# Performance work log

Measured on AMD Instinct MI355X. Metric: run time of the kernel, lower is better.

The kernel has to match this reference:

```python
import jax, jax.numpy as jnp
import numpy as np

B, C_IN, C_OUT = 32, 64, 128
K_SIZE, STRIDE, PAD, H = 3, 1, 1, 56
H_OUT = (H + 2 * PAD - K_SIZE) // STRIDE + 1


def setup_inputs() -> dict:
    key = jax.random.key(0)
    kx, kw = jax.random.split(key)
    x = jax.random.normal(kx, (B, C_IN, H, H), dtype=jnp.float32)
    # kaiming_uniform-ish init for K of shape [kh, kw, C_in, C_out]
    fan_in = K_SIZE * C_IN * C_OUT  # torch fan_in for this layout (dim1 * receptive field)
    bound = np.sqrt(6.0 / fan_in).astype(np.float32)
    K = jax.random.uniform(kw, (K_SIZE, K_SIZE, C_IN, C_OUT), dtype=jnp.float32,
                           minval=-bound, maxval=bound)
    return {"x": x, "K": K}


def reference(x, K):
    # Faithful to the torch code INCLUDING its mismatched flatten orders:
    #   patch flattened as (C_in, kh, kw); K flattened as (kh, kw, C_in).
    xp = jnp.pad(x, ((0, 0), (0, 0), (PAD, PAD), (PAD, PAD)))
    end = (H_OUT - 1) * STRIDE + 1
    # patches[b, c, di, dj, i, j] = xp[b, c, i*stride+di, j*stride+dj]
    rows = []
    for di in range(K_SIZE):
        cols = []
        for dj in range(K_SIZE):
            cols.append(xp[:, :, di:di + end:STRIDE, dj:dj + end:STRIDE])  # [B,C,Ho,Wo]
        rows.append(jnp.stack(cols, axis=2))  # [B,C,kw,Ho,Wo]
    patches = jnp.stack(rows, axis=2)  # [B, C, kh, kw, Ho, Wo]
    # flatten patch in (C, kh, kw) order -> [B, Ho, Wo, C*kh*kw]
    p = patches.transpose(0, 4, 5, 1, 2, 3).reshape(B, H_OUT, H_OUT, -1)
    # K flattened in (kh, kw, C) order, exactly as K.view(-1, out_channels)
    Kf = K.reshape(-1, C_OUT)  # [kh*kw*C_in, C_out]
    out = p @ Kf  # [B, Ho, Wo, C_out]
    return out.transpose(0, 3, 1, 2)  # [B, C_out, Ho, Wo]
```

## Files before the change

kernel.cpp:

```cpp
#include <hip/hip_runtime.h>
#include <hip/hip_bf16.h>
#include <stdint.h>


#define B_   32
#define CIN  64
#define COUT 128
#define H_   56
#define HP   58
#define F_   576

typedef __attribute__((ext_vector_type(8))) short bf16x8;
typedef __attribute__((ext_vector_type(4))) float f32x4;

#define AS1 __attribute__((address_space(1)))
#define AS3 __attribute__((address_space(3)))

#define XP_ELEMS (B_*HP*HP*CIN)
#define XP_SLACK 4096
#define XP_TOTAL (XP_ELEMS + XP_SLACK)
#define WG_ELEMS (COUT*F_)
#define WS_NEEDED ((size_t)(XP_TOTAL + WG_ELEMS) * 2)

#define NROW   (B_*HP)
#define NWBLK  (WG_ELEMS/256)

#define A_BYTES 44544
#define B_OFF   (2*A_BYTES)
#define LDS_TOT (B_OFF + 64*F_*2)

__device__ __forceinline__ int aswz(int tot) {
  return (tot & ~127) | ((tot & 127) ^ (((tot >> 7) & 7) << 4));
}

__global__ __launch_bounds__(256) void prep_all(const float* __restrict__ x,
                                                const float* __restrict__ K,
                                                __hip_bfloat16* __restrict__ xpT,
                                                __hip_bfloat16* __restrict__ WgT) {
  const int id = blockIdx.x;
  const int t  = threadIdx.x;

  if (id > NROW) {
    int n = (id - (NROW + 1))*256 + t;
    int co = n / F_, g = n % F_;
    int di = g / 192, dj = (g % 192) / 64, c = g & 63;
    int f  = c*9 + di*3 + dj;
    int kh = f / 192, kw = (f % 192) / 64, cc = f & 63;
    WgT[n] = __float2bfloat16(K[(((size_t)kh*3 + kw)*CIN + cc)*COUT + co]);
    return;
  }
  if (id == NROW) {
    bf16x8 z = (bf16x8)0;
    for (int idx = t; idx < XP_SLACK/8; idx += 256)
      ((bf16x8*)(xpT + XP_ELEMS))[idx] = z;
    return;
  }

  const int b = id / HP, h = id % HP;
  __hip_bfloat16* orow = xpT + (size_t)(b*HP + h) * HP * CIN;
  if (h == 0 || h == HP-1) {
    bf16x8 z = (bf16x8)0;
    for (int idx = t; idx < HP*CIN/8; idx += 256) ((bf16x8*)orow)[idx] = z;
    return;
  }
  __shared__ __align__(16) float scr[CIN*64];
  const float* xrow = x + ((size_t)(b*CIN)*H_ + (h-1)) * H_;
  for (int idx = t; idx < CIN*14; idx += 256) {
    int c = idx / 14, w4 = idx % 14;
    f32x4 v = *(const f32x4*)(xrow + (size_t)c*(H_*H_) + w4*4);
    *(f32x4*)&scr[c*64 + ((w4 + (c >> 3)) & 15)*4] = v;
  }
  __syncthreads();
  for (int idx = t; idx < HP*8; idx += 256) {
    int wp = idx >> 3, cg = (idx & 7) * 8;
    __align__(16) __hip_bfloat16 tmp[8];
    if (wp == 0 || wp == HP-1) {
#pragma unroll
      for (int k2 = 0; k2 < 8; ++k2) tmp[k2] = __float2bfloat16(0.f);
    } else {
      int w = wp - 1, sl = w >> 2, off = w & 3;
#pragma unroll
      for (int k2 = 0; k2 < 8; ++k2) {
        int c = cg + k2;
        tmp[k2] = __float2bfloat16(scr[c*64 + ((sl + (c >> 3)) & 15)*4 + off]);
      }
    }
    *(bf16x8*)(orow + (size_t)wp*CIN + cg) = *(const bf16x8*)tmp;
  }
}

__global__ __launch_bounds__(256) void conv_mfma(
    const __hip_bfloat16* __restrict__ xpT,
    const __hip_bfloat16* __restrict__ WgT,
    float* __restrict__ out) {
  __shared__ __align__(16) char lds[LDS_TOT];
  const int t    = threadIdx.x;
  const int wave = t >> 6;
  const int l    = t & 63;
  const int lr   = l & 15, lq = l >> 4;
  const int bid  = blockIdx.x;
  const int ch   = bid & 1;
  const int u    = bid >> 1;
  const int m0   = u*4;

  const char* wh = (const char*)WgT + (size_t)(ch*64)*1152;

#pragma unroll
  for (int s = 0; s < 18; ++s) {
    int o  = s*4096 + t*16;
    int co = o / 1152;
    int rb = o - co*1152;
    __builtin_amdgcn_global_load_lds(
        (const AS1 void*)(wh + co*1152 + (rb ^ ((co & 7) << 4))),
        (AS3 void*)(lds + B_OFF + s*4096 + wave*1024), 16, 0, 0);
  }

  auto stageA = [&](int m, char* buf) {
    int bb = m & 31, itile = m >> 5;
    const char* xb = (const char*)xpT +
        (size_t)(bb*HP + itile*4) * HP * CIN * 2;
#pragma unroll
    for (int s = 0; s < 11; ++s) {
      int off = s*4096 + t*16;
      if (off < A_BYTES)
        __builtin_amdgcn_global_load_lds(
            (const AS1 void*)(xb + aswz(off)),
            (AS3 void*)(buf + s*4096 + wave*1024), 16, 0, 0);
    }
  };

  char* Acur = lds;
  char* Anxt = lds + A_BYTES;
  stageA(m0, Acur);
  asm volatile("s_waitcnt vmcnt(0)" ::: "memory");
  __builtin_amdgcn_s_barrier();
  __builtin_amdgcn_sched_barrier(0);

  for (int k = 0; k < 4; ++k) {
    if (k < 3) stageA(m0 + k + 1, Anxt);
    __builtin_amdgcn_sched_barrier(0);

    f32x4 acc[4][4];
#pragma unroll
    for (int mi = 0; mi < 4; ++mi)
#pragma unroll
      for (int ni = 0; ni < 4; ++ni) acc[mi][ni] = (f32x4)0.f;
#pragma unroll
    for (int hc = 0; hc < 18; ++hc) {
      const int kg  = hc*32;
      const int di  = kg / 192;
      const int rem = kg - di*192;
      bf16x8 a[4], bq[4];
#pragma unroll
      for (int mi = 0; mi < 4; ++mi) {
        int tot = ((wave + di)*HP + mi*16 + lr)*128 + rem*2 + lq*16;
        a[mi] = *(const bf16x8*)(Acur + aswz(tot));
      }
      const int kb = hc*64 + lq*16;
#pragma unroll
      for (int ni = 0; ni < 4; ++ni) {
        int co = ni*16 + lr;
        bq[ni] = *(const bf16x8*)(lds + B_OFF + co*1152 + (kb ^ ((co & 7) << 4)));
      }
      __builtin_amdgcn_s_setprio(1);
#pragma unroll
      for (int mi = 0; mi < 4; ++mi)
#pragma unroll
        for (int ni = 0; ni < 4; ++ni)
          acc[mi][ni] = __builtin_amdgcn_mfma_f32_16x16x32_bf16(
              a[mi], bq[ni], acc[mi][ni], 0, 0, 0);
      __builtin_amdgcn_s_setprio(0);
    }
    __builtin_amdgcn_sched_barrier(0);

    {
      int m = m0 + k, bb = m & 31;
      int i = (m >> 5)*4 + wave;
#pragma unroll
      for (int mi = 0; mi < 4; ++mi) {
        int j0 = mi*16 + lq*4;
#pragma unroll
        for (int ni = 0; ni < 4; ++ni) {
          if (j0 < H_) {
            int co = ch*64 + ni*16 + lr;
            float* dst = out + (((size_t)(bb*COUT + co))*H_ + i)*H_ + j0;
            *(f32x4*)dst = acc[mi][ni];
          }
        }
      }
    }
    if (k < 3) {
      asm volatile("s_waitcnt vmcnt(16)" ::: "memory");
      __builtin_amdgcn_s_barrier();
      __builtin_amdgcn_sched_barrier(0);
      char* tmp = Acur; Acur = Anxt; Anxt = tmp;
    }
  }
}

__global__ __launch_bounds__(256) void conv_naive(const float* __restrict__ x,
                                                  const float* __restrict__ K,
                                                  float* __restrict__ out) {
  int idx = blockIdx.x*256 + threadIdx.x;
  const int total = B_*COUT*H_*H_;
  if (idx >= total) return;
  int j = idx % H_, i = (idx / H_) % H_, co = (idx / (H_*H_)) % COUT, b = idx / (H_*H_*COUT);
  float s = 0.f;
  for (int c = 0; c < CIN; ++c)
    for (int di = 0; di < 3; ++di) {
      int ii = i + di - 1;
      if (ii < 0 || ii >= H_) continue;
      for (int dj = 0; dj < 3; ++dj) {
        int jj = j + dj - 1;
        if (jj < 0 || jj >= H_) continue;
        int f = c*9 + di*3 + dj;
        int kh = f / 192, kw = (f % 192) / 64, cc = f & 63;
        s += x[(((size_t)b*CIN + c)*H_ + ii)*H_ + jj] *
             K[(((size_t)kh*3 + kw)*CIN + cc)*COUT + co];
      }
    }
  out[idx] = s;
}

extern "C" void kernel_launch(void* const* d_in, const int* in_sizes, int n_in,
                              void* d_out, int out_size, void* d_ws, size_t ws_size,
                              hipStream_t stream) {
  const float* x = (const float*)d_in[0];
  const float* K = (const float*)d_in[1];
  float* out = (float*)d_out;
  if (ws_size >= WS_NEEDED) {
    __hip_bfloat16* xpT = (__hip_bfloat16*)d_ws;
    __hip_bfloat16* WgT = xpT + XP_TOTAL;
    prep_all<<<NROW + 1 + NWBLK, 256, 0, stream>>>(x, K, xpT, WgT);
    conv_mfma<<<224, 256, 0, stream>>>(xpT, WgT, out);
  } else {
    conv_naive<<<(B_*COUT*H_*H_ + 255)/256, 256, 0, stream>>>(x, K, out);
  }
}
```

Measured before the change: 40.18 us.

## Split conv workgroup into producer and consumer waves, remap block order

The block grows to 512 threads. Four waves now only stream the next input tile into double-buffered LDS with async global-to-LDS loads, and the other four waves only run MFMAs and store outputs, synchronised by one barrier per tile. Block IDs are permuted so that neighbouring blocks fall into groups of 28, and the tile index is recomputed as batch/row-group over 14. The goal is to keep compute waves from stalling on loads, at the cost of doubling the threads per block and adding a full vmcnt wait on the producer side.

```diff
diff --git a/kernel.cpp b/kernel.cpp
--- a/kernel.cpp
+++ b/kernel.cpp
@@ -89,7 +89,7 @@
   }
 }
 
-__global__ __launch_bounds__(256) void conv_mfma(
+__global__ __launch_bounds__(512) void conv_mfma(
     const __hip_bfloat16* __restrict__ xpT,
     const __hip_bfloat16* __restrict__ WgT,
     float* __restrict__ out) {
@@ -98,102 +98,110 @@
   const int wave = t >> 6;
   const int l    = t & 63;
   const int lr   = l & 15, lq = l >> 4;
-  const int bid  = blockIdx.x;
-  const int ch   = bid & 1;
-  const int u    = bid >> 1;
-  const int m0   = u*4;
+
+  const int bid = blockIdx.x;
+  const int sb  = (bid & 7) * 28 + (bid >> 3);
+  const int ch  = sb & 1;
+  const int vg  = sb >> 1;
 
   const char* wh = (const char*)WgT + (size_t)(ch*64)*1152;
 
 #pragma unroll
-  for (int s = 0; s < 18; ++s) {
-    int o  = s*4096 + t*16;
+  for (int s = 0; s < 9; ++s) {
+    int o  = s*8192 + t*16;
     int co = o / 1152;
     int rb = o - co*1152;
     __builtin_amdgcn_global_load_lds(
         (const AS1 void*)(wh + co*1152 + (rb ^ ((co & 7) << 4))),
-        (AS3 void*)(lds + B_OFF + s*4096 + wave*1024), 16, 0, 0);
-  }
-
-  auto stageA = [&](int m, char* buf) {
-    int bb = m & 31, itile = m >> 5;
-    const char* xb = (const char*)xpT +
-        (size_t)(bb*HP + itile*4) * HP * CIN * 2;
+        (AS3 void*)(lds + B_OFF + s*8192 + wave*1024), 16, 0, 0);
+  }
+  if (t >= 256) {
+    const int t2 = t - 256, w2 = wave - 4;
+    const int v = vg*4, bb = v/14, i0 = (v%14)*4;
+    const char* xb = (const char*)xpT + (size_t)(bb*HP + i0) * HP * CIN * 2;
 #pragma unroll
     for (int s = 0; s < 11; ++s) {
-      int off = s*4096 + t*16;
-      if (off < A_BYTES)
+      int o = s*4096 + t2*16;
+      if (o < A_BYTES)
         __builtin_amdgcn_global_load_lds(
-            (const AS1 void*)(xb + aswz(off)),
-            (AS3 void*)(buf + s*4096 + wave*1024), 16, 0, 0);
-    }
-  };
-
-  char* Acur = lds;
-  char* Anxt = lds + A_BYTES;
-  stageA(m0, Acur);
-  asm volatile("s_waitcnt vmcnt(0)" ::: "memory");
-  __builtin_amdgcn_s_barrier();
-  __builtin_amdgcn_sched_barrier(0);
-
-  for (int k = 0; k < 4; ++k) {
-    if (k < 3) stageA(m0 + k + 1, Anxt);
-    __builtin_amdgcn_sched_barrier(0);
-
-    f32x4 acc[4][4];
-#pragma unroll
-    for (int mi = 0; mi < 4; ++mi)
-#pragma unroll
-      for (int ni = 0; ni < 4; ++ni) acc[mi][ni] = (f32x4)0.f;
-#pragma unroll
-    for (int hc = 0; hc < 18; ++hc) {
-      const int kg  = hc*32;
-      const int di  = kg / 192;
-      const int rem = kg - di*192;
-      bf16x8 a[4], bq[4];
-#pragma unroll
-      for (int mi = 0; mi < 4; ++mi) {
-        int tot = ((wave + di)*HP + mi*16 + lr)*128 + rem*2 + lq*16;
-        a[mi] = *(const bf16x8*)(Acur + aswz(tot));
-      }
-      const int kb = hc*64 + lq*16;
-#pragma unroll
-      for (int ni = 0; ni < 4; ++ni) {
-        int co = ni*16 + lr;
-        bq[ni] = *(const bf16x8*)(lds + B_OFF + co*1152 + (kb ^ ((co & 7) << 4)));
-      }
-      __builtin_amdgcn_s_setprio(1);
+            (const AS1 void*)(xb + aswz(o)),
+            (AS3 void*)(lds + s*4096 + w2*1024), 16, 0, 0);
+    }
+  }
+  __syncthreads();
+
+  if (t >= 256) {
+    const int t2 = t - 256, w2 = wave - 4;
+    for (int k = 0; k < 4; ++k) {
+      if (k < 3) {
+        const int v = vg*4 + k + 1, bb = v/14, i0 = (v%14)*4;
+        const char* xb = (const char*)xpT + (size_t)(bb*HP + i0) * HP * CIN * 2;
+        char* Ab = lds + ((k + 1) & 1)*A_BYTES;
+#pragma unroll
+        for (int s = 0; s < 11; ++s) {
+          int o = s*4096 + t2*16;
+          if (o < A_BYTES)
+            __builtin_amdgcn_global_load_lds(
+                (const AS1 void*)(xb + aswz(o)),
+                (AS3 void*)(Ab + s*4096 + w2*1024), 16, 0, 0);
+        }
+        asm volatile("s_waitcnt vmcnt(0)" ::: "memory");
+      }
+      __builtin_amdgcn_s_barrier();
+    }
+  } else {
+    for (int k = 0; k < 4; ++k) {
+      const int v = vg*4 + k, bb = v/14, i0 = (v%14)*4;
+      const char* Ab = lds + (k & 1)*A_BYTES;
+      f32x4 acc[4][4];
 #pragma unroll
       for (int mi = 0; mi < 4; ++mi)
 #pragma unroll
-        for (int ni = 0; ni < 4; ++ni)
-          acc[mi][ni] = __builtin_amdgcn_mfma_f32_16x16x32_bf16(
-              a[mi], bq[ni], acc[mi][ni], 0, 0, 0);
-      __builtin_amdgcn_s_setprio(0);
-    }
-    __builtin_amdgcn_sched_barrier(0);
-
-    {
-      int m = m0 + k, bb = m & 31;
-      int i = (m >> 5)*4 + wave;
+        for (int ni = 0; ni < 4; ++ni) acc[mi][ni] = (f32x4)0.f;
+
+#pragma unroll
+      for (int hc = 0; hc < 18; ++hc) {
+        const int kg  = hc*32;
+        const int di  = kg / 192;
+        const int rem = kg - di*192;
+        bf16x8 a[4], bq[4];
+#pragma unroll
+        for (int mi = 0; mi < 4; ++mi) {
+          int tot = ((wave + di)*HP + mi*16 + lr)*128 + rem*2 + lq*16;
+          a[mi] = *(const bf16x8*)(Ab + aswz(tot));
+        }
+        const int kb = hc*64 + lq*16;
+#pragma unroll
+        for (int ni = 0; ni < 4; ++ni) {
+          int co = ni*16 + lr;
+          bq[ni] = *(const bf16x8*)(lds + B_OFF + co*1152 +
+                                    (kb ^ ((co & 7) << 4)));
+        }
+        __builtin_amdgcn_s_setprio(1);
+#pragma unroll
+        for (int mi = 0; mi < 4; ++mi)
+#pragma unroll
+          for (int ni = 0; ni < 4; ++ni)
+            acc[mi][ni] = __builtin_amdgcn_mfma_f32_16x16x32_bf16(
+                a[mi], bq[ni], acc[mi][ni], 0, 0, 0);
+        __builtin_amdgcn_s_setprio(0);
+      }
+
+      const int i = i0 + wave;
 #pragma unroll
       for (int mi = 0; mi < 4; ++mi) {
         int j0 = mi*16 + lq*4;
-#pragma unroll
-        for (int ni = 0; ni < 4; ++ni) {
-          if (j0 < H_) {
+        if (j0 < H_) {
+#pragma unroll
+          for (int ni = 0; ni < 4; ++ni) {
             int co = ch*64 + ni*16 + lr;
             float* dst = out + (((size_t)(bb*COUT + co))*H_ + i)*H_ + j0;
             *(f32x4*)dst = acc[mi][ni];
           }
         }
       }
-    }
-    if (k < 3) {
-      asm volatile("s_waitcnt vmcnt(16)" ::: "memory");
       __builtin_amdgcn_s_barrier();
       __builtin_amdgcn_sched_barrier(0);
-      char* tmp = Acur; Acur = Anxt; Anxt = tmp;
     }
   }
 }
@@ -232,7 +240,7 @@
     __hip_bfloat16* xpT = (__hip_bfloat16*)d_ws;
     __hip_bfloat16* WgT = xpT + XP_TOTAL;
     prep_all<<<NROW + 1 + NWBLK, 256, 0, stream>>>(x, K, xpT, WgT);
-    conv_mfma<<<224, 256, 0, stream>>>(xpT, WgT, out);
+    conv_mfma<<<224, 512, 0, stream>>>(xpT, WgT, out);
   } else {
     conv_naive<<<(B_*COUT*H_*H_ + 255)/256, 256, 0, stream>>>(x, K, out);
   }
```

Measured after the change: 39.35 us. 1.02x faster.
